# Optimization experiments

Measured on AMD Instinct MI355X. Metric: run time of the kernel, lower is better.

Reference implementation:

```python
import jax, jax.numpy as jnp
import numpy as np
from jax import lax

B, N, D, H, E, K, FF = 4, 1024, 1024, 16, 12, 2, 4
HD = D // H
EPS_LN = 1e-5


def setup_inputs() -> dict:
    key = jax.random.key(0)
    ks = jax.random.split(key, 10)
    s = 0.02
    return {
        "x": jax.random.normal(ks[0], (B, N, D), jnp.float32),
        "Wr": jax.random.normal(ks[1], (E, D), jnp.float32) * s,          # router [E, D] (no bias)
        "Wq": jax.random.normal(ks[2], (E, D, D), jnp.float32) * s,       # per-expert [out, in]
        "Wk": jax.random.normal(ks[3], (E, D, D), jnp.float32) * s,
        "Wv": jax.random.normal(ks[4], (E, D, D), jnp.float32) * s,
        "Wo": jax.random.normal(ks[5], (E, D, D), jnp.float32) * s,
        "W1": jax.random.normal(ks[6], (FF * D, D), jnp.float32) * s,
        "b1": jnp.zeros((FF * D,), jnp.float32),
        "W2": jax.random.normal(ks[7], (D, FF * D), jnp.float32) * s,
        "b2": jnp.zeros((D,), jnp.float32),
        "g1": jnp.ones((D,), jnp.float32),
        "be1": jnp.zeros((D,), jnp.float32),
        "g2": jnp.ones((D,), jnp.float32),
        "be2": jnp.zeros((D,), jnp.float32),
    }


def _ln(x, g, b):
    m = jnp.mean(x, axis=-1, keepdims=True)
    v = jnp.mean(jnp.square(x - m), axis=-1, keepdims=True)
    return (x - m) * lax.rsqrt(v + EPS_LN) * g + b


def _moe_mix(inp, W, combine):
    """sum_e combine[:, e] * (inp @ W[e].T) via scan over the E experts.
    inp: [T, Din], W: [E, Dout, Din], combine: [T, E] -> [T, Dout]"""
    def body(acc, ec):
        We, ce = ec
        return acc + ce[:, None] * (inp @ We.T), None
    acc0 = jnp.zeros((inp.shape[0], W.shape[1]), inp.dtype)
    acc, _ = lax.scan(body, acc0, (W, jnp.swapaxes(combine, 0, 1)))
    return acc


def _moe_attention(x, Wr, Wq, Wk, Wv, Wo):
    x_flat = x.reshape(-1, D)                     # [T, D]
    T = x_flat.shape[0]
    logits = x_flat @ Wr.T                        # [T, E]
    probs = jax.nn.softmax(logits, axis=-1)
    topv, topi = lax.top_k(probs, K)              # [T, K]
    topv = topv / (jnp.sum(topv, axis=-1, keepdims=True) + 1e-6)
    # dense combine weights [T, E] (zero for unselected experts)
    combine = jnp.zeros((T, E), x.dtype).at[jnp.arange(T)[:, None], topi].add(topv)

    q = _moe_mix(x_flat, Wq, combine)
    k = _moe_mix(x_flat, Wk, combine)
    v = _moe_mix(x_flat, Wv, combine)

    # [B, H, N, HD]
    q = q.reshape(B, N, H, HD).transpose(0, 2, 1, 3)
    k = k.reshape(B, N, H, HD).transpose(0, 2, 1, 3)
    v = v.reshape(B, N, H, HD).transpose(0, 2, 1, 3)
    scores = jnp.einsum("bhqd,bhkd->bhqk", q, k) / jnp.sqrt(jnp.asarray(HD, x.dtype))
    attn = jax.nn.softmax(scores, axis=-1)
    out = jnp.einsum("bhqk,bhkd->bhqd", attn, v)
    out_flat = out.transpose(0, 2, 1, 3).reshape(T, D)

    o = _moe_mix(out_flat, Wo, combine)           # expert output projection

    # load-balance loss (no grad in original: computed under torch.no_grad)
    counts = jnp.zeros((E,), x.dtype).at[topi.ravel()].add(1.0)
    p = probs.sum(axis=0)
    lb = jax.lax.stop_gradient((counts / (counts.sum() + 1e-6) * p).sum() * E)
    return o.reshape(B, N, D), lb


def reference(x, Wr, Wq, Wk, Wv, Wo, W1, b1, W2, b2, g1, be1, g2, be2):
    # pre-norm transformer block: x + MoEAttn(LN(x)); + FFN(LN(.))
    attn_out, lb = _moe_attention(_ln(x, g1, be1), Wr, Wq, Wk, Wv, Wo)
    h = x + attn_out
    hn = _ln(h, g2, be2)
    ff = (jax.nn.gelu(hn @ W1.T + b1)) @ W2.T + b2   # dropout=0 (eval)
    y = h + ff
    return y, lb
```

## Files before the change

### kernel.cpp

```cpp
#include <hip/hip_runtime.h>

#define B_ 4
#define N_ 1024
#define D_ 1024
#define H_ 16
#define HD_ 64
#define E_ 12
#define T_ 4096
#define FF_ 4096

static constexpr size_t SZ_ = (size_t)T_ * D_;

typedef __attribute__((ext_vector_type(8))) short bhalf8;
typedef __attribute__((ext_vector_type(4))) float f32x4;

#define GLDS(gp, lp)                                                         \
  __builtin_amdgcn_global_load_lds(                                          \
      (const __attribute__((address_space(1))) void*)(gp),                   \
      (__attribute__((address_space(3))) void*)(lp), 16, 0, 0)

__device__ __forceinline__ float wave_sum64(float v) {
#pragma unroll
  for (int o = 32; o > 0; o >>= 1) v += __shfl_down(v, o);
  return v;
}

__device__ __forceinline__ unsigned short f2bf(float f) {
  unsigned u = __float_as_uint(f);
  u += 0x7FFFu + ((u >> 16) & 1u);
  return (unsigned short)(u >> 16);
}
__device__ __forceinline__ float b2f(unsigned short s) {
  return __uint_as_float(((unsigned)s) << 16);
}
__device__ __forceinline__ unsigned addpair_bf(unsigned x, unsigned y) {
  float lo = b2f((unsigned short)(x & 0xffff)) + b2f((unsigned short)(y & 0xffff));
  float hi = b2f((unsigned short)(x >> 16)) + b2f((unsigned short)(y >> 16));
  return (unsigned)f2bf(lo) | ((unsigned)f2bf(hi) << 16);
}

__device__ __forceinline__ float gelu_f(float x) {
  float u = 0.7978845608028654f * (x + 0.044715f * x * x * x);
  u = fminf(fmaxf(u, -15.f), 15.f);
  float e = __expf(2.f * u);
  float th = (e - 1.f) / (e + 1.f);
  return 0.5f * x * (1.f + th);
}

__device__ __forceinline__ int slot_of(int row, int q) {
  return row * 4 + (q ^ ((row >> 1) & 3));
}

__global__ __launch_bounds__(256) void ln_kernel(const float* __restrict__ x,
    const float* __restrict__ g, const float* __restrict__ b,
    unsigned short* __restrict__ outb) {
  const int t = blockIdx.x, tid = threadIdx.x;
  const size_t base = (size_t)t * D_;
  const float4 v = ((const float4*)(x + base))[tid];
  float s = v.x + v.y + v.z + v.w;
  float s2 = v.x * v.x + v.y * v.y + v.z * v.z + v.w * v.w;
  s = wave_sum64(s);
  s2 = wave_sum64(s2);
  __shared__ float ls[4], ls2[4];
  const int w = tid >> 6;
  if ((tid & 63) == 0) { ls[w] = s; ls2[w] = s2; }
  __syncthreads();
  const float mean = (ls[0] + ls[1] + ls[2] + ls[3]) * (1.0f / D_);
  const float var = (ls2[0] + ls2[1] + ls2[2] + ls2[3]) * (1.0f / D_) - mean * mean;
  const float inv = rsqrtf(var + 1e-5f);
  const float4 gg = ((const float4*)g)[tid];
  const float4 bb = ((const float4*)b)[tid];
  ushort4 u4;
  u4.x = f2bf((v.x - mean) * inv * gg.x + bb.x);
  u4.y = f2bf((v.y - mean) * inv * gg.y + bb.y);
  u4.z = f2bf((v.z - mean) * inv * gg.z + bb.z);
  u4.w = f2bf((v.w - mean) * inv * gg.w + bb.w);
  ((ushort4*)(outb + base))[tid] = u4;
}

__global__ __launch_bounds__(256) void hln2_kernel(const float* __restrict__ x,
    const unsigned short* __restrict__ oa, const unsigned short* __restrict__ ob,
    const float* __restrict__ g, const float* __restrict__ be,
    const float* __restrict__ b2, float* __restrict__ y,
    unsigned short* __restrict__ hnb) {
  const int t = blockIdx.x, tid = threadIdx.x;
  const size_t base = (size_t)t * D_;
  const float4 xv = ((const float4*)(x + base))[tid];
  const ushort4 av = ((const ushort4*)(oa + base))[tid];
  const ushort4 bv = ((const ushort4*)(ob + base))[tid];
  float4 hv;
  hv.x = xv.x + b2f(av.x) + b2f(bv.x);
  hv.y = xv.y + b2f(av.y) + b2f(bv.y);
  hv.z = xv.z + b2f(av.z) + b2f(bv.z);
  hv.w = xv.w + b2f(av.w) + b2f(bv.w);
  const float4 b2v = ((const float4*)b2)[tid];
  float4 yv;
  yv.x = hv.x + b2v.x; yv.y = hv.y + b2v.y;
  yv.z = hv.z + b2v.z; yv.w = hv.w + b2v.w;
  ((float4*)(y + base))[tid] = yv;
  float s = hv.x + hv.y + hv.z + hv.w;
  float s2 = hv.x * hv.x + hv.y * hv.y + hv.z * hv.z + hv.w * hv.w;
  s = wave_sum64(s);
  s2 = wave_sum64(s2);
  __shared__ float ls[4], ls2[4];
  const int w = tid >> 6;
  if ((tid & 63) == 0) { ls[w] = s; ls2[w] = s2; }
  __syncthreads();
  const float mean = (ls[0] + ls[1] + ls[2] + ls[3]) * (1.0f / D_);
  const float var = (ls2[0] + ls2[1] + ls2[2] + ls2[3]) * (1.0f / D_) - mean * mean;
  const float inv = rsqrtf(var + 1e-5f);
  const float4 gg = ((const float4*)g)[tid];
  const float4 bb = ((const float4*)be)[tid];
  ushort4 o4;
  o4.x = f2bf((hv.x - mean) * inv * gg.x + bb.x);
  o4.y = f2bf((hv.y - mean) * inv * gg.y + bb.y);
  o4.z = f2bf((hv.z - mean) * inv * gg.z + bb.z);
  o4.w = f2bf((hv.w - mean) * inv * gg.w + bb.w);
  ((ushort4*)(hnb + base))[tid] = o4;
}

__global__ __launch_bounds__(256) void router_ln(const float* __restrict__ x,
    const float* __restrict__ g, const float* __restrict__ b,
    const float* __restrict__ Wr, float* __restrict__ probs,
    int* __restrict__ topi, float2* __restrict__ topw) {
  const int t = blockIdx.x, tid = threadIdx.x;
  const float4 xv = ((const float4*)(x + (size_t)t * D_))[tid];
  float s = xv.x + xv.y + xv.z + xv.w;
  float s2 = xv.x * xv.x + xv.y * xv.y + xv.z * xv.z + xv.w * xv.w;
  s = wave_sum64(s);
  s2 = wave_sum64(s2);
  __shared__ float ls[4], ls2[4];
  const int w = tid >> 6;
  if ((tid & 63) == 0) { ls[w] = s; ls2[w] = s2; }
  __syncthreads();
  const float mean = (ls[0] + ls[1] + ls[2] + ls[3]) * (1.0f / D_);
  const float var = (ls2[0] + ls2[1] + ls2[2] + ls2[3]) * (1.0f / D_) - mean * mean;
  const float inv = rsqrtf(var + 1e-5f);
  const float4 gg = ((const float4*)g)[tid];
  const float4 bb = ((const float4*)b)[tid];
  float4 xn4;
  xn4.x = (xv.x - mean) * inv * gg.x + bb.x;
  xn4.y = (xv.y - mean) * inv * gg.y + bb.y;
  xn4.z = (xv.z - mean) * inv * gg.z + bb.z;
  xn4.w = (xv.w - mean) * inv * gg.w + bb.w;
  float acc[E_];
#pragma unroll
  for (int e = 0; e < E_; ++e) {
    const float4 wv = ((const float4*)(Wr + (size_t)e * D_))[tid];
    acc[e] = xn4.x * wv.x + xn4.y * wv.y + xn4.z * wv.z + xn4.w * wv.w;
  }
#pragma unroll
  for (int e = 0; e < E_; ++e) acc[e] = wave_sum64(acc[e]);
  __shared__ float red[4][E_];
  if ((tid & 63) == 0) {
#pragma unroll
    for (int e = 0; e < E_; ++e) red[w][e] = acc[e];
  }
  __syncthreads();
  if (tid == 0) {
    float lg[E_];
    float mx = -1e30f;
#pragma unroll
    for (int e = 0; e < E_; ++e) {
      lg[e] = red[0][e] + red[1][e] + red[2][e] + red[3][e];
      mx = fmaxf(mx, lg[e]);
    }
    float p[E_];
    float sum = 0.f;
#pragma unroll
    for (int e = 0; e < E_; ++e) { p[e] = __expf(lg[e] - mx); sum += p[e]; }
    const float invs = 1.f / sum;
#pragma unroll
    for (int e = 0; e < E_; ++e) {
      p[e] *= invs;
      probs[t * E_ + e] = p[e];
    }
    int i0 = 0;
#pragma unroll
    for (int e = 1; e < E_; ++e) if (p[e] > p[i0]) i0 = e;
    int i1 = (i0 == 0) ? 1 : 0;
#pragma unroll
    for (int e = 0; e < E_; ++e) if (e != i0 && p[e] > p[i1]) i1 = e;
    const float rs = 1.f / (p[i0] + p[i1] + 1e-6f);
    topi[t] = i0 | (i1 << 8);
    topw[t] = make_float2(p[i0] * rs, p[i1] * rs);
  }
}

__global__ __launch_bounds__(256) void psum_kernel(const float* __restrict__ probs,
                                                   float* __restrict__ psum) {
  const int tid = threadIdx.x;
  float local[E_] = {};
  for (int t = tid; t < T_; t += 256) {
#pragma unroll
    for (int e = 0; e < E_; ++e) local[e] += probs[t * E_ + e];
  }
#pragma unroll
  for (int e = 0; e < E_; ++e) local[e] = wave_sum64(local[e]);
  __shared__ float red[4][E_];
  const int w = tid >> 6;
  if ((tid & 63) == 0) {
#pragma unroll
    for (int e = 0; e < E_; ++e) red[w][e] = local[e];
  }
  __syncthreads();
  if (tid < E_)
    psum[tid] = red[0][tid] + red[1][tid] + red[2][tid] + red[3][tid];
}

__global__ __launch_bounds__(256) void build_lists(const int* __restrict__ topi,
    const float2* __restrict__ topw, int* __restrict__ ecnt,
    int* __restrict__ etok, float* __restrict__ ewt) {
  const int e = blockIdx.x;
  const int tid = threadIdx.x;
  const int wid = tid >> 6, lane = tid & 63;
  __shared__ int wbase[4];
  __shared__ int base;
  if (tid == 0) base = 0;
  __syncthreads();
  for (int c = 0; c < T_; c += 256) {
    const int t = c + tid;
    const int pk = topi[t];
    const int i0 = pk & 0xFF, i1 = (pk >> 8) & 0xFF;
    const float2 w2 = topw[t];
    const int sel = (i0 == e) ? 0 : ((i1 == e) ? 1 : -1);
    const unsigned long long mask = __ballot(sel >= 0);
    const int prefix = __popcll(mask & ((1ULL << lane) - 1ULL));
    if (lane == 0) wbase[wid] = __popcll(mask);
    __syncthreads();
    if (tid == 0) {
      int s = base;
#pragma unroll
      for (int ww = 0; ww < 4; ++ww) { int cc = wbase[ww]; wbase[ww] = s; s += cc; }
      base = s;
    }
    __syncthreads();
    if (sel >= 0) {
      const int pos = wbase[wid] + prefix;
      etok[e * T_ + pos] = t | (sel << 16);
      ewt[e * T_ + pos] = sel ? w2.y : w2.x;
    }
    __syncthreads();
  }
  if (tid == 0) ecnt[e] = base;
}

__global__ __launch_bounds__(256) void cvtw_kernel(const float* __restrict__ src,
    unsigned short* __restrict__ dst) {
  const size_t i = (size_t)blockIdx.x * 256 + threadIdx.x;
  const float4 v = ((const float4*)src)[i];
  ushort4 o;
  o.x = f2bf(v.x); o.y = f2bf(v.y); o.z = f2bf(v.z); o.w = f2bf(v.w);
  ((ushort4*)dst)[i] = o;
}

__global__ __launch_bounds__(256) void cvtw3_kernel(const float* __restrict__ a,
    const float* __restrict__ b, const float* __restrict__ c,
    unsigned short* __restrict__ dst) {
  const int gw = (E_ * D_ * D_) / 1024;
  const int r = blockIdx.x / gw;
  const int ib = blockIdx.x - r * gw;
  const float* src = (r == 0) ? a : ((r == 1) ? b : c);
  const size_t i = (size_t)ib * 256 + threadIdx.x;
  const float4 v = ((const float4*)src)[i];
  ushort4 o;
  o.x = f2bf(v.x); o.y = f2bf(v.y); o.z = f2bf(v.z); o.w = f2bf(v.w);
  ((ushort4*)(dst + (size_t)r * E_ * D_ * D_))[i] = o;
}

__global__ __launch_bounds__(256) void moe_mfma(const unsigned short* __restrict__ Ab,
    const unsigned short* __restrict__ Wb, unsigned short* __restrict__ outb,
    const int* __restrict__ ecnt, const int* __restrict__ etok,
    const float* __restrict__ ewt) {
  const int e = blockIdx.z;
  const int Me = ecnt[e];
  const int m0 = blockIdx.y * 128;
  if (m0 >= Me) return;
  const int proj = blockIdx.x >> 3;
  const int n0 = (blockIdx.x & 7) * 128;
  const unsigned short* W = Wb + ((size_t)proj * E_ + e) * D_ * D_;
  unsigned short* out = outb + (size_t)proj * 2 * SZ_;
  __shared__ __align__(16) unsigned short As[128 * 32];
  __shared__ __align__(16) unsigned short Bs[128 * 32];
  __shared__ int stok[128];
  __shared__ float swt[128];
  const int tid = threadIdx.x;
  if (tid < 128) {
    const int s = m0 + tid;
    if (s < Me) { stok[tid] = etok[e * T_ + s]; swt[tid] = ewt[e * T_ + s]; }
    else        { stok[tid] = 0;                swt[tid] = 0.f; }
  }
  __syncthreads();
  const int s0 = tid, s1 = tid + 256;
  const int r0 = s0 >> 2, q0 = (s0 & 3) ^ ((r0 >> 1) & 3);
  const int r1 = s1 >> 2, q1 = (s1 & 3) ^ ((r1 >> 1) & 3);
  const unsigned short* aP0 = Ab + (size_t)(stok[r0] & 0xFFFF) * D_ + q0 * 8;
  const unsigned short* aP1 = Ab + (size_t)(stok[r1] & 0xFFFF) * D_ + q1 * 8;
  const unsigned short* bP0 = W + (size_t)(n0 + r0) * D_ + q0 * 8;
  const unsigned short* bP1 = W + (size_t)(n0 + r1) * D_ + q1 * 8;
  char* AsC = (char*)As;
  char* BsC = (char*)Bs;
  const int wave = tid >> 6, lane = tid & 63;
  const int wm0 = (wave >> 1) * 64, wn0 = (wave & 1) * 64;
  const int lr = lane & 15, lq = lane >> 4;
  int aoff[4], boff[4];
#pragma unroll
  for (int t = 0; t < 4; ++t) {
    aoff[t] = slot_of(wm0 + t * 16 + lr, lq) * 16;
    boff[t] = slot_of(wn0 + t * 16 + lr, lq) * 16;
  }
  f32x4 acc[4][4];
#pragma unroll
  for (int i = 0; i < 4; ++i)
#pragma unroll
    for (int j = 0; j < 4; ++j) acc[i][j] = (f32x4){0.f, 0.f, 0.f, 0.f};
  for (int kt = 0; kt < D_; kt += 32) {
    __syncthreads();
    GLDS(aP0 + kt, AsC + s0 * 16);
    GLDS(aP1 + kt, AsC + s1 * 16);
    GLDS(bP0 + kt, BsC + s0 * 16);
    GLDS(bP1 + kt, BsC + s1 * 16);
    __syncthreads();
    bhalf8 af[4], bfr[4];
#pragma unroll
    for (int t = 0; t < 4; ++t) af[t] = *(const bhalf8*)(AsC + aoff[t]);
#pragma unroll
    for (int t = 0; t < 4; ++t) bfr[t] = *(const bhalf8*)(BsC + boff[t]);
#pragma unroll
    for (int i = 0; i < 4; ++i)
#pragma unroll
      for (int j = 0; j < 4; ++j)
        acc[i][j] = __builtin_amdgcn_mfma_f32_16x16x32_bf16(af[i], bfr[j], acc[i][j], 0, 0, 0);
  }
#pragma unroll
  for (int mt = 0; mt < 4; ++mt)
#pragma unroll
    for (int nt = 0; nt < 4; ++nt) {
      const f32x4 c = acc[mt][nt];
      const int col = n0 + wn0 + nt * 16 + lr;
#pragma unroll
      for (int r = 0; r < 4; ++r) {
        const int row = wm0 + mt * 16 + lq * 4 + r;
        if (m0 + row < Me) {
          const int pk = stok[row];
          out[(size_t)(pk >> 16) * SZ_ + (size_t)(pk & 0xFFFF) * D_ + col] =
              f2bf(c[r] * swt[row]);
        }
      }
    }
}

__global__ __launch_bounds__(256) void ffn1_mfma(const unsigned short* __restrict__ Ab,
    const unsigned short* __restrict__ Bb, const float* __restrict__ bias,
    unsigned short* __restrict__ mid) {
  const int m0 = blockIdx.y * 128, n0 = blockIdx.x * 128;
  __shared__ __align__(16) unsigned short As[128 * 32];
  __shared__ __align__(16) unsigned short Bs[128 * 32];
  const int tid = threadIdx.x;
  const int s0 = tid, s1 = tid + 256;
  const int r0 = s0 >> 2, q0 = (s0 & 3) ^ ((r0 >> 1) & 3);
  const int r1 = s1 >> 2, q1 = (s1 & 3) ^ ((r1 >> 1) & 3);
  const unsigned short* aP0 = Ab + (size_t)(m0 + r0) * D_ + q0 * 8;
  const unsigned short* aP1 = Ab + (size_t)(m0 + r1) * D_ + q1 * 8;
  const unsigned short* bP0 = Bb + (size_t)(n0 + r0) * D_ + q0 * 8;
  const unsigned short* bP1 = Bb + (size_t)(n0 + r1) * D_ + q1 * 8;
  char* AsC = (char*)As;
  char* BsC = (char*)Bs;
  const int wave = tid >> 6, lane = tid & 63;
  const int wm0 = (wave >> 1) * 64, wn0 = (wave & 1) * 64;
  const int lr = lane & 15, lq = lane >> 4;
  int aoff[4], boff[4];
#pragma unroll
  for (int t = 0; t < 4; ++t) {
    aoff[t] = slot_of(wm0 + t * 16 + lr, lq) * 16;
    boff[t] = slot_of(wn0 + t * 16 + lr, lq) * 16;
  }
  f32x4 acc[4][4];
#pragma unroll
  for (int i = 0; i < 4; ++i)
#pragma unroll
    for (int j = 0; j < 4; ++j) acc[i][j] = (f32x4){0.f, 0.f, 0.f, 0.f};
  for (int kt = 0; kt < D_; kt += 32) {
    __syncthreads();
    GLDS(aP0 + kt, AsC + s0 * 16);
    GLDS(aP1 + kt, AsC + s1 * 16);
    GLDS(bP0 + kt, BsC + s0 * 16);
    GLDS(bP1 + kt, BsC + s1 * 16);
    __syncthreads();
    bhalf8 af[4], bfr[4];
#pragma unroll
    for (int t = 0; t < 4; ++t) af[t] = *(const bhalf8*)(AsC + aoff[t]);
#pragma unroll
    for (int t = 0; t < 4; ++t) bfr[t] = *(const bhalf8*)(BsC + boff[t]);
#pragma unroll
    for (int i = 0; i < 4; ++i)
#pragma unroll
      for (int j = 0; j < 4; ++j)
        acc[i][j] = __builtin_amdgcn_mfma_f32_16x16x32_bf16(af[i], bfr[j], acc[i][j], 0, 0, 0);
  }
  float bcol[4];
#pragma unroll
  for (int nt = 0; nt < 4; ++nt) bcol[nt] = bias[n0 + wn0 + nt * 16 + lr];
#pragma unroll
  for (int mt = 0; mt < 4; ++mt)
#pragma unroll
    for (int nt = 0; nt < 4; ++nt) {
      const f32x4 c = acc[mt][nt];
      const int col = n0 + wn0 + nt * 16 + lr;
#pragma unroll
      for (int r = 0; r < 4; ++r) {
        const int row = m0 + wm0 + mt * 16 + lq * 4 + r;
        mid[(size_t)row * FF_ + col] = f2bf(gelu_f(c[r] + bcol[nt]));
      }
    }
}

__global__ __launch_bounds__(256) void ffn2_split(const unsigned short* __restrict__ Ab,
    const unsigned short* __restrict__ Bb, float* __restrict__ part0,
    float* __restrict__ part1) {
  const int m0 = blockIdx.y * 128, n0 = blockIdx.x * 128;
  const int k0 = blockIdx.z * (FF_ / 2);
  float* const part = blockIdx.z ? part1 : part0;
  __shared__ __align__(16) unsigned short As[128 * 32];
  __shared__ __align__(16) unsigned short Bs[128 * 32];
  const int tid = threadIdx.x;
  const int s0 = tid, s1 = tid + 256;
  const int r0 = s0 >> 2, q0 = (s0 & 3) ^ ((r0 >> 1) & 3);
  const int r1 = s1 >> 2, q1 = (s1 & 3) ^ ((r1 >> 1) & 3);
  const unsigned short* aP0 = Ab + (size_t)(m0 + r0) * FF_ + q0 * 8 + k0;
  const unsigned short* aP1 = Ab + (size_t)(m0 + r1) * FF_ + q1 * 8 + k0;
  const unsigned short* bP0 = Bb + (size_t)(n0 + r0) * FF_ + q0 * 8 + k0;
  const unsigned short* bP1 = Bb + (size_t)(n0 + r1) * FF_ + q1 * 8 + k0;
  char* AsC = (char*)As;
  char* BsC = (char*)Bs;
  const int wave = tid >> 6, lane = tid & 63;
  const int wm0 = (wave >> 1) * 64, wn0 = (wave & 1) * 64;
  const int lr = lane & 15, lq = lane >> 4;
  int aoff[4], boff[4];
#pragma unroll
  for (int t = 0; t < 4; ++t) {
    aoff[t] = slot_of(wm0 + t * 16 + lr, lq) * 16;
    boff[t] = slot_of(wn0 + t * 16 + lr, lq) * 16;
  }
  f32x4 acc[4][4];
#pragma unroll
  for (int i = 0; i < 4; ++i)
#pragma unroll
    for (int j = 0; j < 4; ++j) acc[i][j] = (f32x4){0.f, 0.f, 0.f, 0.f};
  for (int kt = 0; kt < FF_ / 2; kt += 32) {
    __syncthreads();
    GLDS(aP0 + kt, AsC + s0 * 16);
    GLDS(aP1 + kt, AsC + s1 * 16);
    GLDS(bP0 + kt, BsC + s0 * 16);
    GLDS(bP1 + kt, BsC + s1 * 16);
    __syncthreads();
    bhalf8 af[4], bfr[4];
#pragma unroll
    for (int t = 0; t < 4; ++t) af[t] = *(const bhalf8*)(AsC + aoff[t]);
#pragma unroll
    for (int t = 0; t < 4; ++t) bfr[t] = *(const bhalf8*)(BsC + boff[t]);
#pragma unroll
    for (int i = 0; i < 4; ++i)
#pragma unroll
      for (int j = 0; j < 4; ++j)
        acc[i][j] = __builtin_amdgcn_mfma_f32_16x16x32_bf16(af[i], bfr[j], acc[i][j], 0, 0, 0);
  }
#pragma unroll
  for (int mt = 0; mt < 4; ++mt)
#pragma unroll
    for (int nt = 0; nt < 4; ++nt) {
      const f32x4 c = acc[mt][nt];
      const int col = n0 + wn0 + nt * 16 + lr;
#pragma unroll
      for (int r = 0; r < 4; ++r) {
        const int row = m0 + wm0 + mt * 16 + lq * 4 + r;
        part[(size_t)row * D_ + col] = c[r];
      }
    }
}

__global__ __launch_bounds__(256) void add3_kernel(float* __restrict__ y,
    const float* __restrict__ p0, const float* __restrict__ p1) {
  const size_t i = (size_t)blockIdx.x * 256 + threadIdx.x;
  const float4 a = ((const float4*)y)[i];
  const float4 u = ((const float4*)p0)[i];
  const float4 v = ((const float4*)p1)[i];
  float4 o;
  o.x = a.x + u.x + v.x;
  o.y = a.y + u.y + v.y;
  o.z = a.z + u.z + v.z;
  o.w = a.w + u.w + v.w;
  ((float4*)y)[i] = o;
}

__global__ __launch_bounds__(256) void add2b3_kernel(unsigned short* __restrict__ base) {
  const int reg = blockIdx.x >> 11;
  const int ib = blockIdx.x & 2047;
  unsigned short* a = base + (size_t)reg * 2 * SZ_;
  const unsigned short* b = a + SZ_;
  const size_t i = (size_t)ib * 256 + threadIdx.x;
  uint4 av = ((uint4*)a)[i];
  const uint4 bv = ((const uint4*)b)[i];
  av.x = addpair_bf(av.x, bv.x);
  av.y = addpair_bf(av.y, bv.y);
  av.z = addpair_bf(av.z, bv.z);
  av.w = addpair_bf(av.w, bv.w);
  ((uint4*)a)[i] = av;
}

__global__ __launch_bounds__(256) void attn_kernel(const unsigned short* __restrict__ q,
    const unsigned short* __restrict__ k, const unsigned short* __restrict__ v,
    unsigned short* __restrict__ out) {
  const int bh = blockIdx.x;
  const int b = bh >> 4, h = bh & 15;
  const int q0 = blockIdx.y * 64;
  const int tid = threadIdx.x;
  const int wave = tid >> 6, lane = tid & 63;
  const int lc = lane & 15, lg = lane >> 4;

  __shared__ __align__(16) unsigned short Ks[64 * 64];
  __shared__ __align__(16) unsigned short Vt[64 * 64];
  __shared__ __align__(16) unsigned short Pl[4][16 * 64];
  char* const KsC = (char*)Ks;
  char* const VtC = (char*)Vt;
  char* const PlC = (char*)&Pl[wave][0];

  bhalf8 qf0, qf1;
  {
    const unsigned short* qp =
        q + ((size_t)(b * N_ + q0 + wave * 16 + lc)) * D_ + h * HD_ + lg * 8;
    qf0 = *(const bhalf8*)qp;
    qf1 = *(const bhalf8*)(qp + 32);
  }

  int off[4][2];
#pragma unroll
  for (int t = 0; t < 4; ++t)
#pragma unroll
    for (int ch = 0; ch < 2; ++ch)
      off[t][ch] = (t * 16 + lc) * 128 + (((ch * 4 + lg) ^ (lc & 7)) << 4);

  const int krow = tid >> 2, ks0 = tid & 3;
  const unsigned short* const kgp =
      k + ((size_t)(b * N_ + krow)) * D_ + h * HD_ + ks0 * 8;
  const int kwo0 = krow * 128 + ((ks0 ^ (krow & 7)) << 4);
  const int kwo1 = krow * 128 + (((ks0 ^ 4) ^ (krow & 7)) << 4);
  const int vkv = (tid & 31) * 2, vd0 = (tid >> 5) * 8;
  const unsigned short* const vgp =
      v + ((size_t)(b * N_ + vkv)) * D_ + h * HD_ + vd0;
  int vwo[8];
#pragma unroll
  for (int c = 0; c < 8; ++c) {
    const int d = vd0 + c;
    vwo[c] = d * 128 + ((((vkv >> 3) ^ (d & 7)) << 4)) + (vkv & 7) * 2;
  }

  float m_i[4], l_i[4];
  f32x4 o_acc[4];
#pragma unroll
  for (int r = 0; r < 4; ++r) { m_i[r] = -3.0e38f; l_i[r] = 0.f; }
#pragma unroll
  for (int t = 0; t < 4; ++t) o_acc[t] = (f32x4){0.f, 0.f, 0.f, 0.f};

  uint4 ka = *(const uint4*)(kgp);
  uint4 kb = *(const uint4*)(kgp + 32);
  uint4 va = *(const uint4*)(vgp);
  uint4 vb = *(const uint4*)(vgp + D_);

  for (int kt = 0; kt < 16; ++kt) {
    __syncthreads();
    *(uint4*)(KsC + kwo0) = ka;
    *(uint4*)(KsC + kwo1) = kb;
    {
      const unsigned av4[4] = {va.x, va.y, va.z, va.w};
      const unsigned bv4[4] = {vb.x, vb.y, vb.z, vb.w};
#pragma unroll
      for (int c = 0; c < 4; ++c) {
        const unsigned w0 = (av4[c] & 0xffffu) | (bv4[c] << 16);
        const unsigned w1 = (av4[c] >> 16) | (bv4[c] & 0xffff0000u);
        *(unsigned*)(VtC + vwo[2 * c]) = w0;
        *(unsigned*)(VtC + vwo[2 * c + 1]) = w1;
      }
    }
    __syncthreads();
    if (kt < 15) {
      const size_t go = (size_t)(kt + 1) * 64 * D_;
      ka = *(const uint4*)(kgp + go);
      kb = *(const uint4*)(kgp + go + 32);
      va = *(const uint4*)(vgp + go);
      vb = *(const uint4*)(vgp + go + D_);
    }
    f32x4 s4[4];
#pragma unroll
    for (int t = 0; t < 4; ++t) {
      f32x4 acc = (f32x4){0.f, 0.f, 0.f, 0.f};
      acc = __builtin_amdgcn_mfma_f32_16x16x32_bf16(
          qf0, *(const bhalf8*)(KsC + off[t][0]), acc, 0, 0, 0);
      acc = __builtin_amdgcn_mfma_f32_16x16x32_bf16(
          qf1, *(const bhalf8*)(KsC + off[t][1]), acc, 0, 0, 0);
      s4[t] = acc;
    }
    float alpha[4];
#pragma unroll
    for (int r = 0; r < 4; ++r) {
      const float e0 = s4[0][r] * 0.125f, e1 = s4[1][r] * 0.125f;
      const float e2 = s4[2][r] * 0.125f, e3 = s4[3][r] * 0.125f;
      float mt = fmaxf(fmaxf(e0, e1), fmaxf(e2, e3));
#pragma unroll
      for (int o = 8; o > 0; o >>= 1) mt = fmaxf(mt, __shfl_xor(mt, o));
      const float mn = fmaxf(m_i[r], mt);
      alpha[r] = __expf(m_i[r] - mn);
      m_i[r] = mn;
      const float p0 = __expf(e0 - mn), p1 = __expf(e1 - mn);
      const float p2 = __expf(e2 - mn), p3 = __expf(e3 - mn);
      float rs = p0 + p1 + p2 + p3;
#pragma unroll
      for (int o = 8; o > 0; o >>= 1) rs += __shfl_xor(rs, o);
      l_i[r] = l_i[r] * alpha[r] + rs;
      const int qrow = 4 * lg + r;
      const int rb = qrow * 128 + (lc & 7) * 2;
      const int sw = qrow & 7;
      *(unsigned short*)(PlC + rb + (((0 + (lc >> 3)) ^ sw) << 4)) = f2bf(p0);
      *(unsigned short*)(PlC + rb + (((2 + (lc >> 3)) ^ sw) << 4)) = f2bf(p1);
      *(unsigned short*)(PlC + rb + (((4 + (lc >> 3)) ^ sw) << 4)) = f2bf(p2);
      *(unsigned short*)(PlC + rb + (((6 + (lc >> 3)) ^ sw) << 4)) = f2bf(p3);
    }
#pragma unroll
    for (int t = 0; t < 4; ++t) {
      f32x4 o = o_acc[t];
      o[0] *= alpha[0]; o[1] *= alpha[1]; o[2] *= alpha[2]; o[3] *= alpha[3];
      o_acc[t] = o;
    }
    const bhalf8 pf0 = *(const bhalf8*)(PlC + off[0][0]);
    const bhalf8 pf1 = *(const bhalf8*)(PlC + off[0][1]);
#pragma unroll
    for (int t = 0; t < 4; ++t) {
      o_acc[t] = __builtin_amdgcn_mfma_f32_16x16x32_bf16(
          pf0, *(const bhalf8*)(VtC + off[t][0]), o_acc[t], 0, 0, 0);
      o_acc[t] = __builtin_amdgcn_mfma_f32_16x16x32_bf16(
          pf1, *(const bhalf8*)(VtC + off[t][1]), o_acc[t], 0, 0, 0);
    }
  }
  const size_t obase = ((size_t)(b * N_ + q0 + wave * 16)) * D_ + h * HD_;
#pragma unroll
  for (int r = 0; r < 4; ++r) {
    const float inv = 1.f / l_i[r];
    const size_t rbase = obase + (size_t)(4 * lg + r) * D_;
#pragma unroll
    for (int t = 0; t < 4; ++t)
      out[rbase + t * 16 + lc] = f2bf(o_acc[t][r] * inv);
  }
}

__global__ void lb_kernel(const int* __restrict__ ecnt,
                          const float* __restrict__ psum, float* __restrict__ out) {
  if (threadIdx.x == 0 && blockIdx.x == 0) {
    float tot = 0.f;
    for (int e = 0; e < E_; ++e) tot += (float)ecnt[e];
    float s = 0.f;
    for (int e = 0; e < E_; ++e) s += (float)ecnt[e] / (tot + 1e-6f) * psum[e];
    out[0] = s * (float)E_;
  }
}

extern "C" void kernel_launch(void* const* d_in, const int* in_sizes, int n_in,
                              void* d_out, int out_size, void* d_ws, size_t ws_size,
                              hipStream_t stream) {
  (void)in_sizes; (void)n_in; (void)out_size;
  const float* x  = (const float*)d_in[0];
  const float* Wr = (const float*)d_in[1];
  const float* Wq = (const float*)d_in[2];
  const float* Wk = (const float*)d_in[3];
  const float* Wv = (const float*)d_in[4];
  const float* Wo = (const float*)d_in[5];
  const float* W1 = (const float*)d_in[6];
  const float* b1 = (const float*)d_in[7];
  const float* W2 = (const float*)d_in[8];
  const float* b2 = (const float*)d_in[9];
  const float* g1 = (const float*)d_in[10];
  const float* be1 = (const float*)d_in[11];
  const float* g2 = (const float*)d_in[12];
  const float* be2 = (const float*)d_in[13];
  float* y = (float*)d_out;

  const bool big = ws_size >= (size_t)136 * 1024 * 1024;
  char* p = (char*)d_ws;
  unsigned short *Rb, *xnb, *q2b, *WoB, *W1b, *W2b, *midb;
  char* tail;
  if (big) {
    Rb  = (unsigned short*)p;
    xnb = (unsigned short*)(p + 75497472);
    q2b = (unsigned short*)(p + 75497472 + 8388608);
    tail = p + 75497472 + 8388608 + 6 * SZ_ * 2;
    WoB  = Rb;
    W1b  = (unsigned short*)(p + 25165824);
    W2b  = (unsigned short*)(p + 33554432);
    midb = (unsigned short*)(p + 41943040);
  } else {
    Rb  = (unsigned short*)p;
    xnb = (unsigned short*)(p + 25165824);
    q2b = xnb + SZ_;
    W1b = q2b + 6 * SZ_;
    W2b = W1b + (size_t)FF_ * D_;
    tail = (char*)(W2b + (size_t)FF_ * D_);
    WoB  = Rb;
    midb = (unsigned short*)d_ws;
  }
  unsigned short* k2b = q2b + 2 * SZ_;
  unsigned short* v2b = k2b + 2 * SZ_;
  float* psum = (float*)tail;            tail += E_ * 4;
  int* ecnt = (int*)tail;                tail += E_ * 4;
  int* etok = (int*)tail;                tail += (size_t)E_ * T_ * 4;
  float* ewt = (float*)tail;             tail += (size_t)E_ * T_ * 4;
  float* probs = (float*)tail;           tail += (size_t)T_ * E_ * 4;
  int* topi = (int*)tail;                tail += T_ * 4;
  float2* topw = (float2*)tail;
  unsigned short* attb = v2b + SZ_;
  unsigned short* o2b  = q2b;
  unsigned short* hnb  = v2b;
  float* part0         = (float*)k2b;
  float* part1         = (float*)v2b;

  const int gw = (E_ * D_ * D_) / 1024;
  ln_kernel<<<T_, 256, 0, stream>>>(x, g1, be1, xnb);
  router_ln<<<T_, 256, 0, stream>>>(x, g1, be1, Wr, probs, topi, topw);
  psum_kernel<<<1, 256, 0, stream>>>(probs, psum);
  build_lists<<<E_, 256, 0, stream>>>(topi, topw, ecnt, etok, ewt);
  if (big) {
    cvtw3_kernel<<<3 * gw, 256, 0, stream>>>(Wq, Wk, Wv, Rb);
    moe_mfma<<<dim3(24, T_ / 128, E_), 256, 0, stream>>>(xnb, Rb, q2b, ecnt, etok, ewt);
    cvtw_kernel<<<gw, 256, 0, stream>>>(Wo, WoB);
    cvtw_kernel<<<(FF_ * D_) / 1024, 256, 0, stream>>>(W1, W1b);
    cvtw_kernel<<<(FF_ * D_) / 1024, 256, 0, stream>>>(W2, W2b);
  } else {
    cvtw_kernel<<<(FF_ * D_) / 1024, 256, 0, stream>>>(W1, W1b);
    cvtw_kernel<<<(FF_ * D_) / 1024, 256, 0, stream>>>(W2, W2b);
    cvtw_kernel<<<gw, 256, 0, stream>>>(Wq, Rb);
    moe_mfma<<<dim3(8, T_ / 128, E_), 256, 0, stream>>>(xnb, Rb, q2b, ecnt, etok, ewt);
    cvtw_kernel<<<gw, 256, 0, stream>>>(Wk, Rb);
    moe_mfma<<<dim3(8, T_ / 128, E_), 256, 0, stream>>>(xnb, Rb, k2b, ecnt, etok, ewt);
    cvtw_kernel<<<gw, 256, 0, stream>>>(Wv, Rb);
    moe_mfma<<<dim3(8, T_ / 128, E_), 256, 0, stream>>>(xnb, Rb, v2b, ecnt, etok, ewt);
    cvtw_kernel<<<gw, 256, 0, stream>>>(Wo, Rb);
  }
  add2b3_kernel<<<3 * (SZ_ / 2048), 256, 0, stream>>>(q2b);
  attn_kernel<<<dim3(B_ * H_, N_ / 64), 256, 0, stream>>>(q2b, k2b, v2b, attb);
  moe_mfma<<<dim3(8, T_ / 128, E_), 256, 0, stream>>>(attb, WoB, o2b, ecnt, etok, ewt);
  hln2_kernel<<<T_, 256, 0, stream>>>(x, o2b, o2b + SZ_, g2, be2, b2, y, hnb);
  ffn1_mfma<<<dim3(FF_ / 128, T_ / 128), 256, 0, stream>>>(hnb, W1b, b1, midb);
  ffn2_split<<<dim3(D_ / 128, T_ / 128, 2), 256, 0, stream>>>(midb, W2b, part0, part1);
  add3_kernel<<<SZ_ / 1024, 256, 0, stream>>>(y, part0, part1);
  lb_kernel<<<1, 64, 0, stream>>>(ecnt, psum, y + SZ_);
}
```

Baseline: 627.7 us.

## Double-buffer LDS tiles in MFMA GEMMs to overlap global loads with compute

Converts the three bf16 MFMA GEMM kernels (MoE projection, FFN1, FFN2) from single-buffered LDS tiles with two barriers per k-step to double-buffered tiles with one barrier per k-step. The next tile is prefetched via global_load_lds while the current one feeds the MFMAs. It also raises wave priority around the MFMA block with s_setprio. LDS use per block doubles, which may reduce occupancy. The ordering relies on the single barrier also waiting for the async LDS loads to complete.

New measurement: 624.4 us. About the same (-0.5%).

```diff
diff --git a/kernel.cpp b/kernel.cpp
--- a/kernel.cpp
+++ b/kernel.cpp
@@ -268,6 +268,7 @@
   ((ushort4*)(dst + (size_t)r * E_ * D_ * D_))[i] = o;
 }
 
+
 __global__ __launch_bounds__(256) void moe_mfma(const unsigned short* __restrict__ Ab,
     const unsigned short* __restrict__ Wb, unsigned short* __restrict__ outb,
     const int* __restrict__ ecnt, const int* __restrict__ etok,
@@ -280,8 +281,8 @@
   const int n0 = (blockIdx.x & 7) * 128;
   const unsigned short* W = Wb + ((size_t)proj * E_ + e) * D_ * D_;
   unsigned short* out = outb + (size_t)proj * 2 * SZ_;
-  __shared__ __align__(16) unsigned short As[128 * 32];
-  __shared__ __align__(16) unsigned short Bs[128 * 32];
+  __shared__ __align__(16) unsigned short As[2][128 * 32];
+  __shared__ __align__(16) unsigned short Bs[2][128 * 32];
   __shared__ int stok[128];
   __shared__ float swt[128];
   const int tid = threadIdx.x;
@@ -298,8 +299,10 @@
   const unsigned short* aP1 = Ab + (size_t)(stok[r1] & 0xFFFF) * D_ + q1 * 8;
   const unsigned short* bP0 = W + (size_t)(n0 + r0) * D_ + q0 * 8;
   const unsigned short* bP1 = W + (size_t)(n0 + r1) * D_ + q1 * 8;
-  char* AsC = (char*)As;
-  char* BsC = (char*)Bs;
+  char* const A0 = (char*)As[0];
+  char* const A1 = (char*)As[1];
+  char* const B0 = (char*)Bs[0];
+  char* const B1 = (char*)Bs[1];
   const int wave = tid >> 6, lane = tid & 63;
   const int wm0 = (wave >> 1) * 64, wn0 = (wave & 1) * 64;
   const int lr = lane & 15, lq = lane >> 4;
@@ -314,23 +317,39 @@
   for (int i = 0; i < 4; ++i)
 #pragma unroll
     for (int j = 0; j < 4; ++j) acc[i][j] = (f32x4){0.f, 0.f, 0.f, 0.f};
-  for (int kt = 0; kt < D_; kt += 32) {
-    __syncthreads();
-    GLDS(aP0 + kt, AsC + s0 * 16);
-    GLDS(aP1 + kt, AsC + s1 * 16);
-    GLDS(bP0 + kt, BsC + s0 * 16);
-    GLDS(bP1 + kt, BsC + s1 * 16);
-    __syncthreads();
-    bhalf8 af[4], bfr[4];
-#pragma unroll
-    for (int t = 0; t < 4; ++t) af[t] = *(const bhalf8*)(AsC + aoff[t]);
-#pragma unroll
-    for (int t = 0; t < 4; ++t) bfr[t] = *(const bhalf8*)(BsC + boff[t]);
-#pragma unroll
-    for (int i = 0; i < 4; ++i)
-#pragma unroll
-      for (int j = 0; j < 4; ++j)
-        acc[i][j] = __builtin_amdgcn_mfma_f32_16x16x32_bf16(af[i], bfr[j], acc[i][j], 0, 0, 0);
+  GLDS(aP0, A0 + s0 * 16);
+  GLDS(aP1, A0 + s1 * 16);
+  GLDS(bP0, B0 + s0 * 16);
+  GLDS(bP1, B0 + s1 * 16);
+  __syncthreads();
+  for (int kt = 0; kt < D_; kt += 64) {
+#pragma unroll
+    for (int ph = 0; ph < 2; ++ph) {
+      char* const cA = ph ? A1 : A0;
+      char* const cB = ph ? B1 : B0;
+      char* const nA = ph ? A0 : A1;
+      char* const nB = ph ? B0 : B1;
+      const int kn = kt + 32 + ph * 32;
+      if (kn < D_) {
+        GLDS(aP0 + kn, nA + s0 * 16);
+        GLDS(aP1 + kn, nA + s1 * 16);
+        GLDS(bP0 + kn, nB + s0 * 16);
+        GLDS(bP1 + kn, nB + s1 * 16);
+      }
+      bhalf8 af[4], bfr[4];
+#pragma unroll
+      for (int t = 0; t < 4; ++t) af[t] = *(const bhalf8*)(cA + aoff[t]);
+#pragma unroll
+      for (int t = 0; t < 4; ++t) bfr[t] = *(const bhalf8*)(cB + boff[t]);
+      __builtin_amdgcn_s_setprio(1);
+#pragma unroll
+      for (int i = 0; i < 4; ++i)
+#pragma unroll
+        for (int j = 0; j < 4; ++j)
+          acc[i][j] = __builtin_amdgcn_mfma_f32_16x16x32_bf16(af[i], bfr[j], acc[i][j], 0, 0, 0);
+      __builtin_amdgcn_s_setprio(0);
+      __syncthreads();
+    }
   }
 #pragma unroll
   for (int mt = 0; mt < 4; ++mt)
@@ -354,8 +373,8 @@
     const unsigned short* __restrict__ Bb, const float* __restrict__ bias,
     unsigned short* __restrict__ mid) {
   const int m0 = blockIdx.y * 128, n0 = blockIdx.x * 128;
-  __shared__ __align__(16) unsigned short As[128 * 32];
-  __shared__ __align__(16) unsigned short Bs[128 * 32];
+  __shared__ __align__(16) unsigned short As[2][128 * 32];
+  __shared__ __align__(16) unsigned short Bs[2][128 * 32];
   const int tid = threadIdx.x;
   const int s0 = tid, s1 = tid + 256;
   const int r0 = s0 >> 2, q0 = (s0 & 3) ^ ((r0 >> 1) & 3);
@@ -364,8 +383,10 @@
   const unsigned short* aP1 = Ab + (size_t)(m0 + r1) * D_ + q1 * 8;
   const unsigned short* bP0 = Bb + (size_t)(n0 + r0) * D_ + q0 * 8;
   const unsigned short* bP1 = Bb + (size_t)(n0 + r1) * D_ + q1 * 8;
-  char* AsC = (char*)As;
-  char* BsC = (char*)Bs;
+  char* const A0 = (char*)As[0];
+  char* const A1 = (char*)As[1];
+  char* const B0 = (char*)Bs[0];
+  char* const B1 = (char*)Bs[1];
   const int wave = tid >> 6, lane = tid & 63;
   const int wm0 = (wave >> 1) * 64, wn0 = (wave & 1) * 64;
   const int lr = lane & 15, lq = lane >> 4;
@@ -380,23 +401,39 @@
   for (int i = 0; i < 4; ++i)
 #pragma unroll
     for (int j = 0; j < 4; ++j) acc[i][j] = (f32x4){0.f, 0.f, 0.f, 0.f};
-  for (int kt = 0; kt < D_; kt += 32) {
-    __syncthreads();
-    GLDS(aP0 + kt, AsC + s0 * 16);
-    GLDS(aP1 + kt, AsC + s1 * 16);
-    GLDS(bP0 + kt, BsC + s0 * 16);
-    GLDS(bP1 + kt, BsC + s1 * 16);
-    __syncthreads();
-    bhalf8 af[4], bfr[4];
-#pragma unroll
-    for (int t = 0; t < 4; ++t) af[t] = *(const bhalf8*)(AsC + aoff[t]);
-#pragma unroll
-    for (int t = 0; t < 4; ++t) bfr[t] = *(const bhalf8*)(BsC + boff[t]);
-#pragma unroll
-    for (int i = 0; i < 4; ++i)
-#pragma unroll
-      for (int j = 0; j < 4; ++j)
-        acc[i][j] = __builtin_amdgcn_mfma_f32_16x16x32_bf16(af[i], bfr[j], acc[i][j], 0, 0, 0);
+  GLDS(aP0, A0 + s0 * 16);
+  GLDS(aP1, A0 + s1 * 16);
+  GLDS(bP0, B0 + s0 * 16);
+  GLDS(bP1, B0 + s1 * 16);
+  __syncthreads();
+  for (int kt = 0; kt < D_; kt += 64) {
+#pragma unroll
+    for (int ph = 0; ph < 2; ++ph) {
+      char* const cA = ph ? A1 : A0;
+      char* const cB = ph ? B1 : B0;
+      char* const nA = ph ? A0 : A1;
+      char* const nB = ph ? B0 : B1;
+      const int kn = kt + 32 + ph * 32;
+      if (kn < D_) {
+        GLDS(aP0 + kn, nA + s0 * 16);
+        GLDS(aP1 + kn, nA + s1 * 16);
+        GLDS(bP0 + kn, nB + s0 * 16);
+        GLDS(bP1 + kn, nB + s1 * 16);
+      }
+      bhalf8 af[4], bfr[4];
+#pragma unroll
+      for (int t = 0; t < 4; ++t) af[t] = *(const bhalf8*)(cA + aoff[t]);
+#pragma unroll
+      for (int t = 0; t < 4; ++t) bfr[t] = *(const bhalf8*)(cB + boff[t]);
+      __builtin_amdgcn_s_setprio(1);
+#pragma unroll
+      for (int i = 0; i < 4; ++i)
+#pragma unroll
+        for (int j = 0; j < 4; ++j)
+          acc[i][j] = __builtin_amdgcn_mfma_f32_16x16x32_bf16(af[i], bfr[j], acc[i][j], 0, 0, 0);
+      __builtin_amdgcn_s_setprio(0);
+      __syncthreads();
+    }
   }
   float bcol[4];
 #pragma unroll
@@ -421,8 +458,8 @@
   const int m0 = blockIdx.y * 128, n0 = blockIdx.x * 128;
   const int k0 = blockIdx.z * (FF_ / 2);
   float* const part = blockIdx.z ? part1 : part0;
-  __shared__ __align__(16) unsigned short As[128 * 32];
-  __shared__ __align__(16) unsigned short Bs[128 * 32];
+  __shared__ __align__(16) unsigned short As[2][128 * 32];
+  __shared__ __align__(16) unsigned short Bs[2][128 * 32];
   const int tid = threadIdx.x;
   const int s0 = tid, s1 = tid + 256;
   const int r0 = s0 >> 2, q0 = (s0 & 3) ^ ((r0 >> 1) & 3);
@@ -431,8 +468,10 @@
   const unsigned short* aP1 = Ab + (size_t)(m0 + r1) * FF_ + q1 * 8 + k0;
   const unsigned short* bP0 = Bb + (size_t)(n0 + r0) * FF_ + q0 * 8 + k0;
   const unsigned short* bP1 = Bb + (size_t)(n0 + r1) * FF_ + q1 * 8 + k0;
-  char* AsC = (char*)As;
-  char* BsC = (char*)Bs;
+  char* const A0 = (char*)As[0];
+  char* const A1 = (char*)As[1];
+  char* const B0 = (char*)Bs[0];
+  char* const B1 = (char*)Bs[1];
   const int wave = tid >> 6, lane = tid & 63;
   const int wm0 = (wave >> 1) * 64, wn0 = (wave & 1) * 64;
   const int lr = lane & 15, lq = lane >> 4;
@@ -447,23 +486,39 @@
   for (int i = 0; i < 4; ++i)
 #pragma unroll
     for (int j = 0; j < 4; ++j) acc[i][j] = (f32x4){0.f, 0.f, 0.f, 0.f};
-  for (int kt = 0; kt < FF_ / 2; kt += 32) {
-    __syncthreads();
-    GLDS(aP0 + kt, AsC + s0 * 16);
-    GLDS(aP1 + kt, AsC + s1 * 16);
-    GLDS(bP0 + kt, BsC + s0 * 16);
-    GLDS(bP1 + kt, BsC + s1 * 16);
-    __syncthreads();
-    bhalf8 af[4], bfr[4];
-#pragma unroll
-    for (int t = 0; t < 4; ++t) af[t] = *(const bhalf8*)(AsC + aoff[t]);
-#pragma unroll
-    for (int t = 0; t < 4; ++t) bfr[t] = *(const bhalf8*)(BsC + boff[t]);
-#pragma unroll
-    for (int i = 0; i < 4; ++i)
-#pragma unroll
-      for (int j = 0; j < 4; ++j)
-        acc[i][j] = __builtin_amdgcn_mfma_f32_16x16x32_bf16(af[i], bfr[j], acc[i][j], 0, 0, 0);
+  GLDS(aP0, A0 + s0 * 16);
+  GLDS(aP1, A0 + s1 * 16);
+  GLDS(bP0, B0 + s0 * 16);
+  GLDS(bP1, B0 + s1 * 16);
+  __syncthreads();
+  for (int kt = 0; kt < FF_ / 2; kt += 64) {
+#pragma unroll
+    for (int ph = 0; ph < 2; ++ph) {
+      char* const cA = ph ? A1 : A0;
+      char* const cB = ph ? B1 : B0;
+      char* const nA = ph ? A0 : A1;
+      char* const nB = ph ? B0 : B1;
+      const int kn = kt + 32 + ph * 32;
+      if (kn < FF_ / 2) {
+        GLDS(aP0 + kn, nA + s0 * 16);
+        GLDS(aP1 + kn, nA + s1 * 16);
+        GLDS(bP0 + kn, nB + s0 * 16);
+        GLDS(bP1 + kn, nB + s1 * 16);
+      }
+      bhalf8 af[4], bfr[4];
+#pragma unroll
+      for (int t = 0; t < 4; ++t) af[t] = *(const bhalf8*)(cA + aoff[t]);
+#pragma unroll
+      for (int t = 0; t < 4; ++t) bfr[t] = *(const bhalf8*)(cB + boff[t]);
+      __builtin_amdgcn_s_setprio(1);
+#pragma unroll
+      for (int i = 0; i < 4; ++i)
+#pragma unroll
+        for (int j = 0; j < 4; ++j)
+          acc[i][j] = __builtin_amdgcn_mfma_f32_16x16x32_bf16(af[i], bfr[j], acc[i][j], 0, 0, 0);
+      __builtin_amdgcn_s_setprio(0);
+      __syncthreads();
+    }
   }
 #pragma unroll
   for (int mt = 0; mt < 4; ++mt)
```
